# Performance work log

Hardware: AMD Instinct MI355X
Metric: run time of the kernel (lower is better)

The kernel has to match this reference:

```python
import jax, jax.numpy as jnp
import numpy as np

FEAT_DIM = 128
QUANT_BITS = 2
CODE_BIT = 2
CODE_RANGE = 2 ** CODE_BIT            # 4
N_E = (FEAT_DIM * QUANT_BITS) // CODE_BIT   # 128
EMBED_DIM = N_E * CODE_RANGE          # 512
INTER_DIM = min(4096, EMBED_DIM)      # 512
EPS = 1e-6
LN_EPS = 1e-5
B, S = 8, 8192


def setup_inputs() -> dict:
    key = jax.random.key(0)
    ks = jax.random.split(key, 9)
    x = jax.random.normal(ks[0], (B, S, FEAT_DIM), dtype=jnp.float32)
    # uniform noise for gumbel-softmax (transformed to gumbel inside reference)
    gumbel_u = jax.random.uniform(ks[1], (B, S, N_E, CODE_RANGE), dtype=jnp.float32,
                                  minval=1e-9, maxval=1.0)
    # learned parameters (torch default inits approximated)
    embedding = jax.random.normal(ks[2], (N_E * CODE_BIT, FEAT_DIM), dtype=jnp.float32)
    ln_w = jnp.ones((FEAT_DIM,), jnp.float32)
    ln_b = jnp.zeros((FEAT_DIM,), jnp.float32)
    lim1 = 1.0 / np.sqrt(FEAT_DIM)
    w1 = jax.random.uniform(ks[3], (INTER_DIM, FEAT_DIM), jnp.float32, -lim1, lim1)
    b1 = jax.random.uniform(ks[4], (INTER_DIM,), jnp.float32, -lim1, lim1)
    lim2 = 1.0 / np.sqrt(INTER_DIM)
    w2 = jax.random.uniform(ks[5], (EMBED_DIM, INTER_DIM), jnp.float32, -lim2, lim2)
    b2 = jax.random.uniform(ks[6], (EMBED_DIM,), jnp.float32, -lim2, lim2)
    scale = jnp.ones((FEAT_DIM,), jnp.float32)  # learnable_scale (frozen)
    return {"x": x, "gumbel_u": gumbel_u, "ln_w": ln_w, "ln_b": ln_b,
            "w1": w1, "b1": b1, "w2": w2, "b2": b2,
            "embedding": embedding, "scale": scale}


def _forward(x, gumbel_u, ln_w, ln_b, w1, b1, w2, b2, embedding, scale):
    # ---- encode ----
    x = x / (scale + EPS)
    prescale = jnp.linalg.norm(x, axis=-1, keepdims=True)  # [B,S,1]
    x = x / (prescale + EPS)
    mu = jnp.mean(x, axis=-1, keepdims=True)
    var = jnp.mean(jnp.square(x - mu), axis=-1, keepdims=True)
    x = (x - mu) * jax.lax.rsqrt(var + LN_EPS) * ln_w + ln_b
    h = jax.nn.gelu(jnp.einsum('bsf,if->bsi', x, w1) + b1, approximate=False)
    logits = jnp.einsum('bsi,ei->bse', h, w2) + b2          # [B,S,EMBED_DIM]
    # ---- quantize (gumbel-softmax, tau=1, hard, straight-through) ----
    logits = logits.reshape(B, S, N_E, CODE_RANGE)
    g = -jnp.log(-jnp.log(gumbel_u))
    y = jax.nn.softmax(logits + g, axis=-1)
    hard = jax.nn.one_hot(jnp.argmax(y, axis=-1), CODE_RANGE, dtype=y.dtype)
    code4 = hard + y - jax.lax.stop_gradient(y)             # [B,S,N_E,4]
    code2 = code4[..., :2] + code4[..., 2:3]                # fold class-2 into both bits
    code = code2.reshape(B, S, N_E * CODE_BIT)              # [B,S,256] binary
    # ---- decode ----
    rec = jnp.einsum('bsc,cf->bsf', code, embedding)        # [B,S,FEAT_DIM]
    postscale = jnp.linalg.norm(rec, axis=-1, keepdims=True)
    rec = rec / (postscale + EPS) * (prescale + EPS) * (scale + EPS)
    return rec


def reference(x, gumbel_u, ln_w, ln_b, w1, b1, w2, b2, embedding, scale):
    return _forward(x, gumbel_u, ln_w, ln_b, w1, b1, w2, b2, embedding, scale)
```

## Files before the change

kernel.cpp:

```cpp
#include <hip/hip_runtime.h>
#include <math.h>

#define FEAT  128
#define INTER 512
#define EMB   512
#define TB    64

typedef short s16x8 __attribute__((ext_vector_type(8)));
typedef float f32x4 __attribute__((ext_vector_type(4)));

static constexpr float F_EPS    = 1e-6f;
static constexpr float F_LN_EPS = 1e-5f;

#define MFMA(a,b,c) __builtin_amdgcn_mfma_f32_16x16x32_bf16(a,b,c,0,0,0)

#define W1BASE 0
#define W2BASE 196608
#define EBASE  983040

__device__ __forceinline__ unsigned short f2bf(float f) {
    union { float f; unsigned u; } v; v.f = f;
    unsigned r = v.u + 0x7FFFu + ((v.u >> 16) & 1u);
    return (unsigned short)(r >> 16);
}
__device__ __forceinline__ float bf2f(unsigned short h) {
    union { unsigned u; float f; } v; v.u = ((unsigned)h) << 16;
    return v.f;
}
__device__ __forceinline__ void split3(float x, unsigned short& h,
                                       unsigned short& m, unsigned short& l) {
    h = f2bf(x);
    float r1 = x - bf2f(h);
    m = f2bf(r1);
    l = f2bf(r1 - bf2f(m));
}
__device__ __forceinline__ float gelu_exact(float v) {
    return 0.5f * v * (1.0f + erff(v * 0.70710678118654752440f));
}

__global__ __launch_bounds__(256) void vc_pack(const float* __restrict__ w1,
                                               const float* __restrict__ w2,
                                               const float* __restrict__ emb,
                                               unsigned short* __restrict__ P) {
    int id = blockIdx.x * 256 + threadIdx.x;
    int fid = id >> 6, l = id & 63;
    if (fid >= 704) return;
    int lr = l & 15, lq = l >> 4;
    float v[8];
    size_t dst;
    int three = 1;
    if (fid < 128) {
        int kt = fid >> 5, nt = fid & 31;
        const float* s = w1 + (size_t)(nt * 16 + lr) * FEAT + kt * 32 + 8 * lq;
        #pragma unroll
        for (int i = 0; i < 8; ++i) v[i] = s[i];
        dst = W1BASE + (size_t)fid * 1536;
    } else if (fid < 640) {
        int f2 = fid - 128, kt = f2 >> 5, nt = f2 & 31;
        const float* s = w2 + (size_t)(nt * 16 + lr) * INTER + kt * 32 + 8 * lq;
        #pragma unroll
        for (int i = 0; i < 8; ++i) v[i] = s[i];
        dst = W2BASE + (size_t)f2 * 1536;
    } else {
        int f3 = fid - 640, kt = f3 >> 3, nt = f3 & 7;
        #pragma unroll
        for (int i = 0; i < 8; ++i)
            v[i] = emb[(size_t)(kt * 32 + 8 * lq + i) * FEAT + nt * 16 + lr];
        dst = EBASE + (size_t)f3 * 1024;
        three = 0;
    }
    s16x8 vh, vm, vl;
    #pragma unroll
    for (int i = 0; i < 8; ++i) {
        unsigned short a, b, c;
        split3(v[i], a, b, c);
        vh[i] = (short)a; vm[i] = (short)b; vl[i] = (short)c;
    }
    *(s16x8*)(P + dst + l * 8)       = vh;
    *(s16x8*)(P + dst + 512 + l * 8) = vm;
    if (three) *(s16x8*)(P + dst + 1024 + l * 8) = vl;
}

__global__ __launch_bounds__(1024) void vc_fused(
    const float* __restrict__ x,   const float* __restrict__ gu,
    const float* __restrict__ lnw, const float* __restrict__ lnb,
    const float* __restrict__ b1,  const float* __restrict__ b2,
    const float* __restrict__ scl, const unsigned short* __restrict__ wsP,
    float* __restrict__ out)
{
    __shared__ __align__(16) unsigned char smem[158208];
    unsigned short* sXn = (unsigned short*)smem;
    unsigned short* sH  = (unsigned short*)(smem + 49152);
    unsigned*       sC  = (unsigned*)(smem + 147456);
    float*          sPre  = (float*)(smem + 155648);
    float*          sPart = (float*)(smem + 155904);
    float*          sFac  = (float*)(smem + 157952);

    const int tid = threadIdx.x;
    const int w  = tid >> 6;
    const int l  = tid & 63;
    const int lr = l & 15, lq = l >> 4;
    const long tok0 = (long)blockIdx.x * TB;

    {
        const int t = tid >> 4;
        const int q = tid & 15;
        const float* xr = x + (tok0 + t) * FEAT + q * 8;
        float v[8];
        #pragma unroll
        for (int k = 0; k < 8; ++k) v[k] = xr[k] / (scl[q * 8 + k] + F_EPS);
        float ss = 0.f;
        #pragma unroll
        for (int k = 0; k < 8; ++k) ss += v[k] * v[k];
        ss += __shfl_xor(ss, 1); ss += __shfl_xor(ss, 2);
        ss += __shfl_xor(ss, 4); ss += __shfl_xor(ss, 8);
        const float pre = sqrtf(ss);
        if (q == 0) sPre[t] = pre;
        const float ip = 1.0f / (pre + F_EPS);
        #pragma unroll
        for (int k = 0; k < 8; ++k) v[k] *= ip;
        float sm = 0.f;
        #pragma unroll
        for (int k = 0; k < 8; ++k) sm += v[k];
        sm += __shfl_xor(sm, 1); sm += __shfl_xor(sm, 2);
        sm += __shfl_xor(sm, 4); sm += __shfl_xor(sm, 8);
        const float mu = sm * (1.0f / 128.0f);
        float vv = 0.f;
        #pragma unroll
        for (int k = 0; k < 8; ++k) { float d = v[k] - mu; vv += d * d; }
        vv += __shfl_xor(vv, 1); vv += __shfl_xor(vv, 2);
        vv += __shfl_xor(vv, 4); vv += __shfl_xor(vv, 8);
        const float rst = 1.0f / sqrtf(vv * (1.0f / 128.0f) + F_LN_EPS);

        const int mt  = t >> 4;
        const int kt  = q >> 2;
        const int sub = q & 3;
        const size_t base = ((size_t)(mt * 4 + kt) * 64 + (t & 15) + 16 * sub) * 8;
        s16x8 vh, vm, vlo;
        #pragma unroll
        for (int i = 0; i < 8; ++i) {
            const float xnv = (v[i] - mu) * rst * lnw[q * 8 + i] + lnb[q * 8 + i];
            unsigned short a, b, c;
            split3(xnv, a, b, c);
            vh[i] = (short)a; vm[i] = (short)b; vlo[i] = (short)c;
        }
        *(s16x8*)(sXn + base)         = vh;
        *(s16x8*)(sXn + 8192 + base)  = vm;
        *(s16x8*)(sXn + 16384 + base) = vlo;
    }
    __syncthreads();

    f32x4 acc2[4][2];
    #pragma unroll
    for (int m = 0; m < 4; ++m)
        #pragma unroll
        for (int n = 0; n < 2; ++n)
            #pragma unroll
            for (int r = 0; r < 4; ++r) acc2[m][n][r] = 0.f;

    for (int half = 0; half < 2; ++half) {
        f32x4 acc1[4];
        #pragma unroll
        for (int m = 0; m < 4; ++m)
            #pragma unroll
            for (int r = 0; r < 4; ++r) acc1[m][r] = 0.f;

        #pragma unroll
        for (int kt = 0; kt < 4; ++kt) {
            s16x8 A[4][3];
            #pragma unroll
            for (int m = 0; m < 4; ++m) {
                const size_t base = ((size_t)(m * 4 + kt) * 64 + l) * 8;
                A[m][0] = *(const s16x8*)(sXn + base);
                A[m][1] = *(const s16x8*)(sXn + 8192 + base);
                A[m][2] = *(const s16x8*)(sXn + 16384 + base);
            }
            const int nt = half * 16 + w;
            const unsigned short* bp = wsP + W1BASE + (size_t)(kt * 32 + nt) * 1536 + l * 8;
            const s16x8 bh = *(const s16x8*)bp;
            const s16x8 bm = *(const s16x8*)(bp + 512);
            const s16x8 bl = *(const s16x8*)(bp + 1024);
            #pragma unroll
            for (int m = 0; m < 4; ++m) {
                f32x4 c = acc1[m];
                c = MFMA(A[m][1], bm, c);
                c = MFMA(A[m][2], bh, c);
                c = MFMA(A[m][0], bl, c);
                c = MFMA(A[m][1], bh, c);
                c = MFMA(A[m][0], bm, c);
                c = MFMA(A[m][0], bh, c);
                acc1[m] = c;
            }
        }

        {
            const float b1v = b1[half * 256 + w * 16 + lr];
            #pragma unroll
            for (int m = 0; m < 4; ++m)
                #pragma unroll
                for (int r = 0; r < 4; ++r) {
                    const float h = gelu_exact(acc1[m][r] + b1v);
                    unsigned short hh, hm, hl;
                    split3(h, hh, hm, hl);
                    const int tokr = 4 * lq + r;
                    const int row  = m * 16 + tokr;
                    const int nl   = w * 16 + lr;
                    const int gsw  = (nl >> 3) ^ (tokr & 7);
                    const size_t off = (size_t)row * 256 + gsw * 8 + (nl & 7);
                    sH[off]          = hh;
                    sH[16384 + off]  = hm;
                    sH[32768 + off]  = hl;
                }
        }
        __syncthreads();

        for (int kk = 0; kk < 8; ++kk) {
            s16x8 A[4][3];
            #pragma unroll
            for (int m = 0; m < 4; ++m) {
                const int row = m * 16 + lr;
                const int gsw = (kk * 4 + lq) ^ (lr & 7);
                const size_t off = (size_t)row * 256 + (size_t)gsw * 8;
                A[m][0] = *(const s16x8*)(sH + off);
                A[m][1] = *(const s16x8*)(sH + 16384 + off);
                A[m][2] = *(const s16x8*)(sH + 32768 + off);
            }
            #pragma unroll
            for (int ntl = 0; ntl < 2; ++ntl) {
                const int fid2 = (half * 8 + kk) * 32 + (w * 2 + ntl);
                const unsigned short* bp = wsP + W2BASE + (size_t)fid2 * 1536 + l * 8;
                const s16x8 bh = *(const s16x8*)bp;
                const s16x8 bm = *(const s16x8*)(bp + 512);
                const s16x8 bl = *(const s16x8*)(bp + 1024);
                #pragma unroll
                for (int m = 0; m < 4; ++m) {
                    f32x4 c = acc2[m][ntl];
                    c = MFMA(A[m][1], bm, c);
                    c = MFMA(A[m][2], bh, c);
                    c = MFMA(A[m][0], bl, c);
                    c = MFMA(A[m][1], bh, c);
                    c = MFMA(A[m][0], bm, c);
                    c = MFMA(A[m][0], bh, c);
                    acc2[m][ntl] = c;
                }
            }
        }
        __syncthreads();
    }

    {
        float b2v[2];
        #pragma unroll
        for (int ntl = 0; ntl < 2; ++ntl) b2v[ntl] = b2[w * 32 + ntl * 16 + lr];
        const int qq  = lr >> 2;
        const int cls = l & 3;
        #pragma unroll
        for (int m = 0; m < 4; ++m)
            #pragma unroll
            for (int ntl = 0; ntl < 2; ++ntl) {
                #pragma unroll
                for (int r = 0; r < 4; ++r) {
                    const long tg = tok0 + m * 16 + 4 * lq + r;
                    const float u = gu[tg * 512 + w * 32 + ntl * 16 + lr];
                    float v = acc2[m][ntl][r] + b2v[ntl] - logf(-logf(u));
                    int   ci = cls;
                    float v1 = __shfl_xor(v, 1); int c1 = __shfl_xor(ci, 1);
                    if (v1 > v || (v1 == v && c1 < ci)) { v = v1; ci = c1; }
                    float v2 = __shfl_xor(v, 2); int c2 = __shfl_xor(ci, 2);
                    if (v2 > v || (v2 == v && c2 < ci)) { v = v2; ci = c2; }
                    if (cls == 0) {
                        const int row = m * 16 + 4 * lq + r;
                        const int col = (w * 2 + ntl) ^ ((row & 7) << 2);
                        ((unsigned char*)(sC + row * 32 + col))[qq] = (unsigned char)ci;
                    }
                }
            }
    }
    __syncthreads();

    const int nt_d = w & 7;
    const int mp   = w >> 3;
    f32x4 accd[2];
    #pragma unroll
    for (int mi = 0; mi < 2; ++mi)
        #pragma unroll
        for (int r = 0; r < 4; ++r) accd[mi][r] = 0.f;

    #pragma unroll
    for (int kt = 0; kt < 8; ++kt) {
        const unsigned short* bp = wsP + EBASE + (size_t)(kt * 8 + nt_d) * 1024 + l * 8;
        const s16x8 bh = *(const s16x8*)bp;
        const s16x8 bl = *(const s16x8*)(bp + 512);
        #pragma unroll
        for (int mi = 0; mi < 2; ++mi) {
            const int row = (mp * 2 + mi) * 16 + lr;
            const int col = (kt * 4 + lq) ^ ((row & 7) << 2);
            const unsigned cw = sC[row * 32 + col];
            s16x8 a;
            #pragma unroll
            for (int q2 = 0; q2 < 4; ++q2) {
                const unsigned c = (cw >> (8 * q2)) & 0xffu;
                a[2 * q2]     = ((c & 1u) == 0u) ? (short)0x3F80 : (short)0;
                a[2 * q2 + 1] = (((c + 1u) & 2u) != 0u) ? (short)0x3F80 : (short)0;
            }
            accd[mi] = MFMA(a, bh, accd[mi]);
            accd[mi] = MFMA(a, bl, accd[mi]);
        }
    }
    __syncthreads();

    {
        #pragma unroll
        for (int mi = 0; mi < 2; ++mi) {
            float ps[4];
            #pragma unroll
            for (int r = 0; r < 4; ++r) {
                float s = accd[mi][r] * accd[mi][r];
                s += __shfl_xor(s, 1); s += __shfl_xor(s, 2);
                s += __shfl_xor(s, 4); s += __shfl_xor(s, 8);
                ps[r] = s;
            }
            if (lr == 0)
                *(float4*)(sPart + nt_d * 64 + (mp * 2 + mi) * 16 + 4 * lq) =
                    make_float4(ps[0], ps[1], ps[2], ps[3]);
        }
    }
    __syncthreads();
    if (tid < 64) {
        float ssum = 0.f;
        #pragma unroll
        for (int g = 0; g < 8; ++g) ssum += sPart[g * 64 + tid];
        const float post = sqrtf(ssum);
        sFac[tid] = (1.0f / (post + F_EPS)) * (sPre[tid] + F_EPS);
    }
    __syncthreads();
    {
        const float sclv = scl[nt_d * 16 + lr] + F_EPS;
        #pragma unroll
        for (int mi = 0; mi < 2; ++mi)
            #pragma unroll
            for (int r = 0; r < 4; ++r) {
                const int tokr = (mp * 2 + mi) * 16 + 4 * lq + r;
                const float o = accd[mi][r] * sFac[tokr] * sclv;
                out[(tok0 + tokr) * FEAT + nt_d * 16 + lr] = o;
            }
    }
}

extern "C" void kernel_launch(void* const* d_in, const int* in_sizes, int n_in,
                              void* d_out, int out_size, void* d_ws, size_t ws_size,
                              hipStream_t stream) {
    const float* x   = (const float*)d_in[0];
    const float* gu  = (const float*)d_in[1];
    const float* lnw = (const float*)d_in[2];
    const float* lnb = (const float*)d_in[3];
    const float* w1  = (const float*)d_in[4];
    const float* b1  = (const float*)d_in[5];
    const float* w2  = (const float*)d_in[6];
    const float* b2  = (const float*)d_in[7];
    const float* emb = (const float*)d_in[8];
    const float* scl = (const float*)d_in[9];
    float* out = (float*)d_out;

    unsigned short* wsP = (unsigned short*)d_ws;

    hipLaunchKernelGGL(vc_pack, dim3(176), dim3(256), 0, stream, w1, w2, emb, wsP);

    const int ntok = in_sizes[0] / FEAT;
    hipLaunchKernelGGL(vc_fused, dim3(ntok / TB), dim3(1024), 0, stream,
                       x, gu, lnw, lnb, b1, b2, scl, wsP, out);
}
```

Measured before the change: 373.2 us.

## Halve token block to 32 to cut LDS and allow two blocks per CU

Token tile per block drops from 64 to 32, halving shared memory (about 79KB) and per-wave accumulator registers, with launch bounds requesting more occupancy. With 160KB LDS on the CU this could let two 1024-thread blocks co-reside and overlap phases. The cost is that each block reloads the full W1/W2/embedding B-fragments from global for half as many tokens, doubling weight traffic and L2 pressure. Only half the threads do the normalization phase.

```diff
diff --git a/kernel.cpp b/kernel.cpp
--- a/kernel.cpp
+++ b/kernel.cpp
@@ -4,7 +4,7 @@
 #define FEAT  128
 #define INTER 512
 #define EMB   512
-#define TB    64
+#define TB    32
 
 typedef short s16x8 __attribute__((ext_vector_type(8)));
 typedef float f32x4 __attribute__((ext_vector_type(4)));
@@ -81,20 +81,20 @@
     if (three) *(s16x8*)(P + dst + 1024 + l * 8) = vl;
 }
 
-__global__ __launch_bounds__(1024) void vc_fused(
+__global__ __launch_bounds__(1024, 8) void vc_fused(
     const float* __restrict__ x,   const float* __restrict__ gu,
     const float* __restrict__ lnw, const float* __restrict__ lnb,
     const float* __restrict__ b1,  const float* __restrict__ b2,
     const float* __restrict__ scl, const unsigned short* __restrict__ wsP,
     float* __restrict__ out)
 {
-    __shared__ __align__(16) unsigned char smem[158208];
+    __shared__ __align__(16) unsigned char smem[79104];
     unsigned short* sXn = (unsigned short*)smem;
-    unsigned short* sH  = (unsigned short*)(smem + 49152);
-    unsigned*       sC  = (unsigned*)(smem + 147456);
-    float*          sPre  = (float*)(smem + 155648);
-    float*          sPart = (float*)(smem + 155904);
-    float*          sFac  = (float*)(smem + 157952);
+    unsigned short* sH  = (unsigned short*)(smem + 24576);
+    unsigned*       sC  = (unsigned*)(smem + 73728);
+    float*          sPre  = (float*)(smem + 77824);
+    float*          sPart = (float*)(smem + 77952);
+    float*          sFac  = (float*)(smem + 78976);
 
     const int tid = threadIdx.x;
     const int w  = tid >> 6;
@@ -102,7 +102,7 @@
     const int lr = l & 15, lq = l >> 4;
     const long tok0 = (long)blockIdx.x * TB;
 
-    {
+    if (tid < 512) {
         const int t = tid >> 4;
         const int q = tid & 15;
         const float* xr = x + (tok0 + t) * FEAT + q * 8;
@@ -144,36 +144,36 @@
             split3(xnv, a, b, c);
             vh[i] = (short)a; vm[i] = (short)b; vlo[i] = (short)c;
         }
-        *(s16x8*)(sXn + base)         = vh;
-        *(s16x8*)(sXn + 8192 + base)  = vm;
-        *(s16x8*)(sXn + 16384 + base) = vlo;
-    }
-    __syncthreads();
-
-    f32x4 acc2[4][2];
+        *(s16x8*)(sXn + base)        = vh;
+        *(s16x8*)(sXn + 4096 + base) = vm;
+        *(s16x8*)(sXn + 8192 + base) = vlo;
+    }
+    __syncthreads();
+
+    f32x4 acc2[2][2];
     #pragma unroll
-    for (int m = 0; m < 4; ++m)
+    for (int m = 0; m < 2; ++m)
         #pragma unroll
         for (int n = 0; n < 2; ++n)
             #pragma unroll
             for (int r = 0; r < 4; ++r) acc2[m][n][r] = 0.f;
 
     for (int half = 0; half < 2; ++half) {
-        f32x4 acc1[4];
-        #pragma unroll
-        for (int m = 0; m < 4; ++m)
+        f32x4 acc1[2];
+        #pragma unroll
+        for (int m = 0; m < 2; ++m)
             #pragma unroll
             for (int r = 0; r < 4; ++r) acc1[m][r] = 0.f;
 
         #pragma unroll
         for (int kt = 0; kt < 4; ++kt) {
-            s16x8 A[4][3];
-            #pragma unroll
-            for (int m = 0; m < 4; ++m) {
+            s16x8 A[2][3];
+            #pragma unroll
+            for (int m = 0; m < 2; ++m) {
                 const size_t base = ((size_t)(m * 4 + kt) * 64 + l) * 8;
                 A[m][0] = *(const s16x8*)(sXn + base);
-                A[m][1] = *(const s16x8*)(sXn + 8192 + base);
-                A[m][2] = *(const s16x8*)(sXn + 16384 + base);
+                A[m][1] = *(const s16x8*)(sXn + 4096 + base);
+                A[m][2] = *(const s16x8*)(sXn + 8192 + base);
             }
             const int nt = half * 16 + w;
             const unsigned short* bp = wsP + W1BASE + (size_t)(kt * 32 + nt) * 1536 + l * 8;
@@ -181,7 +181,7 @@
             const s16x8 bm = *(const s16x8*)(bp + 512);
             const s16x8 bl = *(const s16x8*)(bp + 1024);
             #pragma unroll
-            for (int m = 0; m < 4; ++m) {
+            for (int m = 0; m < 2; ++m) {
                 f32x4 c = acc1[m];
                 c = MFMA(A[m][1], bm, c);
                 c = MFMA(A[m][2], bh, c);
@@ -196,7 +196,7 @@
         {
             const float b1v = b1[half * 256 + w * 16 + lr];
             #pragma unroll
-            for (int m = 0; m < 4; ++m)
+            for (int m = 0; m < 2; ++m)
                 #pragma unroll
                 for (int r = 0; r < 4; ++r) {
                     const float h = gelu_exact(acc1[m][r] + b1v);
@@ -208,22 +208,22 @@
                     const int gsw  = (nl >> 3) ^ (tokr & 7);
                     const size_t off = (size_t)row * 256 + gsw * 8 + (nl & 7);
                     sH[off]          = hh;
-                    sH[16384 + off]  = hm;
-                    sH[32768 + off]  = hl;
+                    sH[8192 + off]   = hm;
+                    sH[16384 + off]  = hl;
                 }
         }
         __syncthreads();
 
         for (int kk = 0; kk < 8; ++kk) {
-            s16x8 A[4][3];
-            #pragma unroll
-            for (int m = 0; m < 4; ++m) {
+            s16x8 A[2][3];
+            #pragma unroll
+            for (int m = 0; m < 2; ++m) {
                 const int row = m * 16 + lr;
                 const int gsw = (kk * 4 + lq) ^ (lr & 7);
                 const size_t off = (size_t)row * 256 + (size_t)gsw * 8;
                 A[m][0] = *(const s16x8*)(sH + off);
-                A[m][1] = *(const s16x8*)(sH + 16384 + off);
-                A[m][2] = *(const s16x8*)(sH + 32768 + off);
+                A[m][1] = *(const s16x8*)(sH + 8192 + off);
+                A[m][2] = *(const s16x8*)(sH + 16384 + off);
             }
             #pragma unroll
             for (int ntl = 0; ntl < 2; ++ntl) {
@@ -233,7 +233,7 @@
                 const s16x8 bm = *(const s16x8*)(bp + 512);
                 const s16x8 bl = *(const s16x8*)(bp + 1024);
                 #pragma unroll
-                for (int m = 0; m < 4; ++m) {
+                for (int m = 0; m < 2; ++m) {
                     f32x4 c = acc2[m][ntl];
                     c = MFMA(A[m][1], bm, c);
                     c = MFMA(A[m][2], bh, c);
@@ -255,7 +255,7 @@
         const int qq  = lr >> 2;
         const int cls = l & 3;
         #pragma unroll
-        for (int m = 0; m < 4; ++m)
+        for (int m = 0; m < 2; ++m)
             #pragma unroll
             for (int ntl = 0; ntl < 2; ++ntl) {
                 #pragma unroll
@@ -280,56 +280,48 @@
 
     const int nt_d = w & 7;
     const int mp   = w >> 3;
-    f32x4 accd[2];
+    f32x4 accd;
     #pragma unroll
-    for (int mi = 0; mi < 2; ++mi)
-        #pragma unroll
-        for (int r = 0; r < 4; ++r) accd[mi][r] = 0.f;
+    for (int r = 0; r < 4; ++r) accd[r] = 0.f;
 
     #pragma unroll
     for (int kt = 0; kt < 8; ++kt) {
         const unsigned short* bp = wsP + EBASE + (size_t)(kt * 8 + nt_d) * 1024 + l * 8;
         const s16x8 bh = *(const s16x8*)bp;
         const s16x8 bl = *(const s16x8*)(bp + 512);
-        #pragma unroll
-        for (int mi = 0; mi < 2; ++mi) {
-            const int row = (mp * 2 + mi) * 16 + lr;
-            const int col = (kt * 4 + lq) ^ ((row & 7) << 2);
-            const unsigned cw = sC[row * 32 + col];
-            s16x8 a;
-            #pragma unroll
-            for (int q2 = 0; q2 < 4; ++q2) {
-                const unsigned c = (cw >> (8 * q2)) & 0xffu;
-                a[2 * q2]     = ((c & 1u) == 0u) ? (short)0x3F80 : (short)0;
-                a[2 * q2 + 1] = (((c + 1u) & 2u) != 0u) ? (short)0x3F80 : (short)0;
-            }
-            accd[mi] = MFMA(a, bh, accd[mi]);
-            accd[mi] = MFMA(a, bl, accd[mi]);
-        }
+        const int row = mp * 16 + lr;
+        const int col = (kt * 4 + lq) ^ ((row & 7) << 2);
+        const unsigned cw = sC[row * 32 + col];
+        s16x8 a;
+        #pragma unroll
+        for (int q2 = 0; q2 < 4; ++q2) {
+            const unsigned c = (cw >> (8 * q2)) & 0xffu;
+            a[2 * q2]     = ((c & 1u) == 0u) ? (short)0x3F80 : (short)0;
+            a[2 * q2 + 1] = (((c + 1u) & 2u) != 0u) ? (short)0x3F80 : (short)0;
+        }
+        accd = MFMA(a, bh, accd);
+        accd = MFMA(a, bl, accd);
     }
     __syncthreads();
 
     {
-        #pragma unroll
-        for (int mi = 0; mi < 2; ++mi) {
-            float ps[4];
-            #pragma unroll
-            for (int r = 0; r < 4; ++r) {
-                float s = accd[mi][r] * accd[mi][r];
-                s += __shfl_xor(s, 1); s += __shfl_xor(s, 2);
-                s += __shfl_xor(s, 4); s += __shfl_xor(s, 8);
-                ps[r] = s;
-            }
-            if (lr == 0)
-                *(float4*)(sPart + nt_d * 64 + (mp * 2 + mi) * 16 + 4 * lq) =
-                    make_float4(ps[0], ps[1], ps[2], ps[3]);
-        }
-    }
-    __syncthreads();
-    if (tid < 64) {
+        float ps[4];
+        #pragma unroll
+        for (int r = 0; r < 4; ++r) {
+            float s = accd[r] * accd[r];
+            s += __shfl_xor(s, 1); s += __shfl_xor(s, 2);
+            s += __shfl_xor(s, 4); s += __shfl_xor(s, 8);
+            ps[r] = s;
+        }
+        if (lr == 0)
+            *(float4*)(sPart + nt_d * 32 + mp * 16 + 4 * lq) =
+                make_float4(ps[0], ps[1], ps[2], ps[3]);
+    }
+    __syncthreads();
+    if (tid < 32) {
         float ssum = 0.f;
         #pragma unroll
-        for (int g = 0; g < 8; ++g) ssum += sPart[g * 64 + tid];
+        for (int g = 0; g < 8; ++g) ssum += sPart[g * 32 + tid];
         const float post = sqrtf(ssum);
         sFac[tid] = (1.0f / (post + F_EPS)) * (sPre[tid] + F_EPS);
     }
@@ -337,13 +329,11 @@
     {
         const float sclv = scl[nt_d * 16 + lr] + F_EPS;
         #pragma unroll
-        for (int mi = 0; mi < 2; ++mi)
-            #pragma unroll
-            for (int r = 0; r < 4; ++r) {
-                const int tokr = (mp * 2 + mi) * 16 + 4 * lq + r;
-                const float o = accd[mi][r] * sFac[tokr] * sclv;
-                out[(tok0 + tokr) * FEAT + nt_d * 16 + lr] = o;
-            }
+        for (int r = 0; r < 4; ++r) {
+            const int tokr = mp * 16 + 4 * lq + r;
+            const float o = accd[r] * sFac[tokr] * sclv;
+            out[(tok0 + tokr) * FEAT + nt_d * 16 + lr] = o;
+        }
     }
 }
 
```

After: 336.9 us. 9.7% less time.
